# Kernel tuning notes

Measured on AMD Instinct MI355X. Metric: run time of the kernel, lower is better.

The kernel has to match this reference:

```python
import jax, jax.numpy as jnp
import numpy as np

B, P, D, H = 2048, 128, 64, 8
DB = 10  # D_obs + D_pos = 7 + 3, hard-coded in the module


def setup_inputs() -> dict:
    key = jax.random.key(0)
    ks = jax.random.split(key, 10)
    s = lambda fan_in: 1.0 / np.sqrt(fan_in)
    return {
        "x": jax.random.normal(ks[0], (B, D), dtype=jnp.float32),
        "b": jax.random.normal(ks[1], (B, P, DB), dtype=jnp.float32),
        "W_kvx": jax.random.uniform(ks[2], (D, 2 * H * D), jnp.float32, -s(D), s(D)),
        "b_kvx": jax.random.uniform(ks[3], (2 * H * D,), jnp.float32, -s(D), s(D)),
        "W_kvb": jax.random.uniform(ks[4], (DB, 2 * H * D), jnp.float32, -s(DB), s(DB)),
        "b_kvb": jax.random.uniform(ks[5], (2 * H * D,), jnp.float32, -s(DB), s(DB)),
        "W_q": jax.random.uniform(ks[6], (D, H * D), jnp.float32, -s(D), s(D)),
        "b_q": jax.random.uniform(ks[7], (H * D,), jnp.float32, -s(D), s(D)),
        "W_f": jax.random.uniform(ks[8], (H * D, D), jnp.float32, -s(H * D), s(H * D)),
        "b_f": jax.random.uniform(ks[9], (D,), jnp.float32, -s(H * D), s(H * D)),
    }


def reference(x, b, W_kvx, b_kvx, W_kvb, b_kvb, W_q, b_q, W_f, b_f):
    Bn, Dx = x.shape
    _, Pn, _ = b.shape
    # dual projections + broadcast add: [B,1,2HD] + [B,P,2HD]
    kv = (x @ W_kvx + b_kvx)[:, None, :] + (jnp.einsum('bpe,ef->bpf', b, W_kvb) + b_kvb)
    k, v = jnp.split(kv, 2, axis=-1)            # each [B,P,H*D]
    k = k.reshape(Bn, Pn, H, Dx)
    v = v.reshape(Bn, Pn, H, Dx)
    q = (x @ W_q + b_q).reshape(Bn, H, Dx)
    dots = jnp.einsum('bphd,bhd->bph', k, q) / np.sqrt(Dx).astype(np.float32)
    # NOTE: faithful to source — softmax over the HEAD axis (last dim of [B,P,H])
    attn = jax.nn.softmax(dots, axis=-1)
    vals = jnp.einsum('bph,bphd->bhd', attn, v)  # sum over positions P
    out = vals.reshape(Bn, H * Dx) @ W_f + b_f
    return out
```

## Files before the change

kernel.cpp:

```cpp
#include <hip/hip_runtime.h>

#define NDB 10

__global__ __launch_bounds__(256) void proj_kernel(
    const float* __restrict__ x, const float* __restrict__ W_kvx,
    const float* __restrict__ b_kvx, const float* __restrict__ b_kvb,
    const float* __restrict__ W_q, const float* __restrict__ b_q,
    float* __restrict__ XQ)
{
    __shared__ float x_t[64][68];
    const int t = threadIdx.x;
    const int row0 = blockIdx.x * 64;
    const int ct = blockIdx.y;

    {
        const int r = t & 63, kb = (t >> 6) * 16;
        float4 xv[4];
        #pragma unroll
        for (int i = 0; i < 4; ++i)
            xv[i] = *(const float4*)&x[(size_t)(row0 + r) * 64 + kb + i * 4];
        #pragma unroll
        for (int i = 0; i < 4; ++i) {
            x_t[kb + i * 4 + 0][r] = xv[i].x;
            x_t[kb + i * 4 + 1][r] = xv[i].y;
            x_t[kb + i * 4 + 2][r] = xv[i].z;
            x_t[kb + i * 4 + 3][r] = xv[i].w;
        }
    }
    __syncthreads();

    const bool iskv = (ct < 16);
    const int c0 = (iskv ? ct * 64 : (ct - 16) * 64) + (t & 15) * 4;
    const int stride = iskv ? 1024 : 512;
    const float* Wp = (iskv ? W_kvx : W_q) + c0;
    const int r0 = (t >> 4) * 4;

    float acc[4][4] = {};
    #pragma unroll 8
    for (int k = 0; k < 64; ++k) {
        float4 a  = *(const float4*)&x_t[k][r0];
        float4 wv = *(const float4*)&Wp[k * stride];
        float av[4] = {a.x, a.y, a.z, a.w};
        float wvv[4] = {wv.x, wv.y, wv.z, wv.w};
        #pragma unroll
        for (int i = 0; i < 4; ++i)
            #pragma unroll
            for (int jj = 0; jj < 4; ++jj)
                acc[i][jj] = fmaf(av[i], wvv[jj], acc[i][jj]);
    }
    float4 bias;
    if (iskv) {
        float4 b1 = *(const float4*)&b_kvx[c0];
        float4 b2 = *(const float4*)&b_kvb[c0];
        bias.x = b1.x + b2.x; bias.y = b1.y + b2.y;
        bias.z = b1.z + b2.z; bias.w = b1.w + b2.w;
    } else {
        bias = *(const float4*)&b_q[c0];
    }
    const int outcol = ct * 64 + (t & 15) * 4;
    #pragma unroll
    for (int i = 0; i < 4; ++i) {
        float4 o;
        o.x = acc[i][0] + bias.x; o.y = acc[i][1] + bias.y;
        o.z = acc[i][2] + bias.z; o.w = acc[i][3] + bias.w;
        *(float4*)&XQ[(size_t)(row0 + r0 + i) * 1536 + outcol] = o;
    }
}

__global__ __launch_bounds__(256) void attn_core(
    const float* __restrict__ bmat, const float* __restrict__ W_kvb,
    const float* __restrict__ XQ, float* __restrict__ VALS)
{
    __shared__ float bb_s[4][128][11];
    __shared__ float q_s[4][8][68];
    __shared__ float dot0_s[4][8];
    __shared__ float Wqkb_s[4][NDB][8];
    __shared__ float A_s[4][8];
    __shared__ float S_s[4][NDB][8];

    const int t = threadIdx.x, lane = t & 63, w = t >> 6;
    const int row = blockIdx.x * 4 + w;
    const float* __restrict__ xq = XQ + (size_t)row * 1536;

    {
        float4 a  = *(const float4*)&xq[1024 + lane * 4];
        float4 b4 = *(const float4*)&xq[1024 + 256 + lane * 4];
        int d0 = lane * 4;
        float av[4] = {a.x, a.y, a.z, a.w};
        float bv[4] = {b4.x, b4.y, b4.z, b4.w};
        #pragma unroll
        for (int c = 0; c < 4; ++c) {
            int d = d0 + c;
            q_s[w][d >> 6][d & 63] = av[c];
            int d2 = d + 256;
            q_s[w][d2 >> 6][d2 & 63] = bv[c];
        }
    }
    {
        const float* bsrc = bmat + (size_t)row * 1280;
        #pragma unroll
        for (int i = 0; i < 20; ++i) {
            int idx = lane + 64 * i;
            bb_s[w][idx / 10][idx % 10] = bsrc[idx];
        }
    }

    const int h = lane >> 3, i8 = lane & 7;
    {
        float s = 0.f;
        #pragma unroll
        for (int j = 0; j < 8; ++j) {
            int d = i8 + 8 * j;
            s = fmaf(xq[h * 64 + d], q_s[w][h][d], s);
        }
        s += __shfl_xor(s, 1); s += __shfl_xor(s, 2); s += __shfl_xor(s, 4);
        if (i8 == 0) dot0_s[w][h] = s;
    }
    #pragma unroll
    for (int e = 0; e < NDB; ++e) {
        float s = 0.f;
        #pragma unroll
        for (int m = 0; m < 8; ++m) {
            int d = i8 + 8 * m;
            s = fmaf(W_kvb[e * 1024 + h * 64 + d], q_s[w][h][d], s);
        }
        s += __shfl_xor(s, 1); s += __shfl_xor(s, 2); s += __shfl_xor(s, 4);
        if (i8 == 0) Wqkb_s[w][e][h] = s;
    }

    {
        const int hh = lane & 7, pg = lane >> 3;
        float aA = 0.f, aS[NDB];
        #pragma unroll
        for (int e = 0; e < NDB; ++e) aS[e] = 0.f;
        float wq[NDB];
        #pragma unroll
        for (int e = 0; e < NDB; ++e) wq[e] = Wqkb_s[w][e][hh];
        const float d0v = dot0_s[w][hh];
        #pragma unroll 4
        for (int it = 0; it < 16; ++it) {
            int p = pg + 8 * it;
            float bbv[NDB];
            #pragma unroll
            for (int e = 0; e < NDB; ++e) bbv[e] = bb_s[w][p][e];
            float dot = d0v;
            #pragma unroll
            for (int e = 0; e < NDB; ++e) dot = fmaf(bbv[e], wq[e], dot);
            dot *= 0.125f;
            float m = dot;
            m = fmaxf(m, __shfl_xor(m, 1));
            m = fmaxf(m, __shfl_xor(m, 2));
            m = fmaxf(m, __shfl_xor(m, 4));
            float ex = __expf(dot - m);
            float sum = ex;
            sum += __shfl_xor(sum, 1); sum += __shfl_xor(sum, 2); sum += __shfl_xor(sum, 4);
            float at = ex * __builtin_amdgcn_rcpf(sum);
            aA += at;
            #pragma unroll
            for (int e = 0; e < NDB; ++e) aS[e] = fmaf(at, bbv[e], aS[e]);
        }
        aA += __shfl_xor(aA, 8); aA += __shfl_xor(aA, 16); aA += __shfl_xor(aA, 32);
        #pragma unroll
        for (int e = 0; e < NDB; ++e) {
            aS[e] += __shfl_xor(aS[e], 8);
            aS[e] += __shfl_xor(aS[e], 16);
            aS[e] += __shfl_xor(aS[e], 32);
        }
        if (pg == 0) {
            A_s[w][hh] = aA;
            #pragma unroll
            for (int e = 0; e < NDB; ++e) S_s[w][e][hh] = aS[e];
        }
    }

    #pragma unroll
    for (int i = 0; i < 8; ++i) {
        int f = lane + 64 * i;
        float v = A_s[w][i] * xq[512 + f];
        #pragma unroll
        for (int e = 0; e < NDB; ++e)
            v = fmaf(S_s[w][e][i], W_kvb[e * 1024 + 512 + f], v);
        VALS[(size_t)row * 512 + f] = v;
    }
}

__global__ __launch_bounds__(256) void out_kernel(
    const float* __restrict__ VALS, const float* __restrict__ W_f,
    const float* __restrict__ b_f, float* __restrict__ out)
{
    __shared__ float wf_s[128][64];
    const int t = threadIdx.x, j = t & 63;
    const int row = blockIdx.x * 4 + (t >> 6);
    const int rowU = __builtin_amdgcn_readfirstlane(row);
    const float4* vrow = (const float4*)(VALS + (size_t)rowU * 512);

    float acc = 0.f;
    #pragma unroll
    for (int kt = 0; kt < 4; ++kt) {
        __syncthreads();
        #pragma unroll
        for (int i = 0; i < 8; ++i) {
            int fi = t + 256 * i;
            ((float4*)wf_s)[fi] = ((const float4*)(W_f + kt * 128 * 64))[fi];
        }
        __syncthreads();
        #pragma unroll 8
        for (int k4 = 0; k4 < 32; ++k4) {
            float4 v = vrow[kt * 32 + k4];
            int k = k4 * 4;
            acc = fmaf(v.x, wf_s[k + 0][j], acc);
            acc = fmaf(v.y, wf_s[k + 1][j], acc);
            acc = fmaf(v.z, wf_s[k + 2][j], acc);
            acc = fmaf(v.w, wf_s[k + 3][j], acc);
        }
    }
    out[(size_t)row * 64 + j] = acc + b_f[j];
}

extern "C" void kernel_launch(void* const* d_in, const int* in_sizes, int n_in,
                              void* d_out, int out_size, void* d_ws, size_t ws_size,
                              hipStream_t stream)
{
    const float* x     = (const float*)d_in[0];
    const float* bmat  = (const float*)d_in[1];
    const float* W_kvx = (const float*)d_in[2];
    const float* b_kvx = (const float*)d_in[3];
    const float* W_kvb = (const float*)d_in[4];
    const float* b_kvb = (const float*)d_in[5];
    const float* W_q   = (const float*)d_in[6];
    const float* b_q   = (const float*)d_in[7];
    const float* W_f   = (const float*)d_in[8];
    const float* b_f   = (const float*)d_in[9];
    float* out  = (float*)d_out;
    float* XQ   = (float*)d_ws;
    float* VALS = XQ + (size_t)2048 * 1536;

    proj_kernel<<<dim3(32, 24), 256, 0, stream>>>(x, W_kvx, b_kvx, b_kvb, W_q, b_q, XQ);
    attn_core<<<512, 256, 0, stream>>>(bmat, W_kvb, XQ, VALS);
    out_kernel<<<512, 256, 0, stream>>>(VALS, W_f, b_f, out);
}
```

Measured before the change: 131.6 us.

## Fuse output projection into attention kernel with one batch row per block

Merges out_kernel into attn_core, so VALS stays in shared memory instead of making a global write/read round trip, and one kernel launch goes away. Each block now handles a single batch row using all four wavefronts cooperatively: positions are split across waves, partial sums are reduced through shared memory, and the W_f GEMV is split over the K dimension with a final cross-wave sum. In exchange it adds several block-wide barriers, launches four times as many blocks, and reads W_f directly from global/cache for every row instead of staging it in LDS.

Result: faster. 109.2 us (-17.1%).

```diff
diff --git a/kernel.cpp b/kernel.cpp
--- a/kernel.cpp
+++ b/kernel.cpp
@@ -69,80 +69,80 @@
 
 __global__ __launch_bounds__(256) void attn_core(
     const float* __restrict__ bmat, const float* __restrict__ W_kvb,
-    const float* __restrict__ XQ, float* __restrict__ VALS)
+    const float* __restrict__ XQ, const float* __restrict__ W_f,
+    const float* __restrict__ b_f, float* __restrict__ out)
 {
-    __shared__ float bb_s[4][128][11];
-    __shared__ float q_s[4][8][68];
-    __shared__ float dot0_s[4][8];
-    __shared__ float Wqkb_s[4][NDB][8];
-    __shared__ float A_s[4][8];
-    __shared__ float S_s[4][NDB][8];
+    __shared__ float bb_s[128][11];
+    __shared__ float q_s[8][68];
+    __shared__ float dot0_s[8];
+    __shared__ float Wqkb_s[NDB][8];
+    __shared__ float partA[4][8];
+    __shared__ float partS[4][NDB][8];
+    __shared__ float A_s[8];
+    __shared__ float S_s[NDB][8];
+    __shared__ float vals_s[512];
+    __shared__ float pout[4][64];
 
     const int t = threadIdx.x, lane = t & 63, w = t >> 6;
-    const int row = blockIdx.x * 4 + w;
+    const int row = blockIdx.x;
     const float* __restrict__ xq = XQ + (size_t)row * 1536;
 
     {
-        float4 a  = *(const float4*)&xq[1024 + lane * 4];
-        float4 b4 = *(const float4*)&xq[1024 + 256 + lane * 4];
-        int d0 = lane * 4;
-        float av[4] = {a.x, a.y, a.z, a.w};
-        float bv[4] = {b4.x, b4.y, b4.z, b4.w};
-        #pragma unroll
-        for (int c = 0; c < 4; ++c) {
-            int d = d0 + c;
-            q_s[w][d >> 6][d & 63] = av[c];
-            int d2 = d + 256;
-            q_s[w][d2 >> 6][d2 & 63] = bv[c];
-        }
-    }
-    {
         const float* bsrc = bmat + (size_t)row * 1280;
         #pragma unroll
-        for (int i = 0; i < 20; ++i) {
-            int idx = lane + 64 * i;
-            bb_s[w][idx / 10][idx % 10] = bsrc[idx];
-        }
-    }
-
-    const int h = lane >> 3, i8 = lane & 7;
-    {
-        float s = 0.f;
-        #pragma unroll
-        for (int j = 0; j < 8; ++j) {
-            int d = i8 + 8 * j;
-            s = fmaf(xq[h * 64 + d], q_s[w][h][d], s);
-        }
-        s += __shfl_xor(s, 1); s += __shfl_xor(s, 2); s += __shfl_xor(s, 4);
-        if (i8 == 0) dot0_s[w][h] = s;
-    }
-    #pragma unroll
-    for (int e = 0; e < NDB; ++e) {
-        float s = 0.f;
-        #pragma unroll
-        for (int m = 0; m < 8; ++m) {
-            int d = i8 + 8 * m;
-            s = fmaf(W_kvb[e * 1024 + h * 64 + d], q_s[w][h][d], s);
-        }
-        s += __shfl_xor(s, 1); s += __shfl_xor(s, 2); s += __shfl_xor(s, 4);
-        if (i8 == 0) Wqkb_s[w][e][h] = s;
-    }
+        for (int i = 0; i < 5; ++i) {
+            int idx = t + 256 * i;
+            bb_s[idx / 10][idx % 10] = bsrc[idx];
+        }
+        float qa = xq[1024 + t];
+        float qb = xq[1024 + 256 + t];
+        q_s[t >> 6][t & 63] = qa;
+        q_s[(t + 256) >> 6][t & 63] = qb;
+        float p1 = xq[t] * qa;
+        float p2 = xq[t + 256] * qb;
+        #pragma unroll
+        for (int m = 1; m <= 32; m <<= 1) p1 += __shfl_xor(p1, m);
+        #pragma unroll
+        for (int m = 1; m <= 32; m <<= 1) p2 += __shfl_xor(p2, m);
+        if (lane == 0) { dot0_s[w] = p1; dot0_s[w + 4] = p2; }
+    }
+    __syncthreads();
+
+    {
+        const int g = t >> 3, l = t & 7;
+        #pragma unroll
+        for (int ro = 0; ro < 3; ++ro) {
+            int o = g + 32 * ro;
+            if (o < 80) {
+                int e = o >> 3, h = o & 7;
+                float s = 0.f;
+                #pragma unroll
+                for (int m = 0; m < 8; ++m) {
+                    int d = l + 8 * m;
+                    s = fmaf(W_kvb[e * 1024 + h * 64 + d], q_s[h][d], s);
+                }
+                s += __shfl_xor(s, 1); s += __shfl_xor(s, 2); s += __shfl_xor(s, 4);
+                if (l == 0) Wqkb_s[e][h] = s;
+            }
+        }
+    }
+    __syncthreads();
 
     {
         const int hh = lane & 7, pg = lane >> 3;
+        float wq[NDB];
+        #pragma unroll
+        for (int e = 0; e < NDB; ++e) wq[e] = Wqkb_s[e][hh];
+        const float d0v = dot0_s[hh];
         float aA = 0.f, aS[NDB];
         #pragma unroll
         for (int e = 0; e < NDB; ++e) aS[e] = 0.f;
-        float wq[NDB];
-        #pragma unroll
-        for (int e = 0; e < NDB; ++e) wq[e] = Wqkb_s[w][e][hh];
-        const float d0v = dot0_s[w][hh];
-        #pragma unroll 4
-        for (int it = 0; it < 16; ++it) {
-            int p = pg + 8 * it;
+        #pragma unroll
+        for (int it = 0; it < 4; ++it) {
+            int p = w * 32 + pg + 8 * it;
             float bbv[NDB];
             #pragma unroll
-            for (int e = 0; e < NDB; ++e) bbv[e] = bb_s[w][p][e];
+            for (int e = 0; e < NDB; ++e) bbv[e] = bb_s[p][e];
             float dot = d0v;
             #pragma unroll
             for (int e = 0; e < NDB; ++e) dot = fmaf(bbv[e], wq[e], dot);
@@ -167,54 +167,53 @@
             aS[e] += __shfl_xor(aS[e], 32);
         }
         if (pg == 0) {
-            A_s[w][hh] = aA;
-            #pragma unroll
-            for (int e = 0; e < NDB; ++e) S_s[w][e][hh] = aS[e];
-        }
-    }
-
-    #pragma unroll
-    for (int i = 0; i < 8; ++i) {
-        int f = lane + 64 * i;
-        float v = A_s[w][i] * xq[512 + f];
-        #pragma unroll
-        for (int e = 0; e < NDB; ++e)
-            v = fmaf(S_s[w][e][i], W_kvb[e * 1024 + 512 + f], v);
-        VALS[(size_t)row * 512 + f] = v;
-    }
-}
-
-__global__ __launch_bounds__(256) void out_kernel(
-    const float* __restrict__ VALS, const float* __restrict__ W_f,
-    const float* __restrict__ b_f, float* __restrict__ out)
-{
-    __shared__ float wf_s[128][64];
-    const int t = threadIdx.x, j = t & 63;
-    const int row = blockIdx.x * 4 + (t >> 6);
-    const int rowU = __builtin_amdgcn_readfirstlane(row);
-    const float4* vrow = (const float4*)(VALS + (size_t)rowU * 512);
-
-    float acc = 0.f;
-    #pragma unroll
-    for (int kt = 0; kt < 4; ++kt) {
-        __syncthreads();
-        #pragma unroll
-        for (int i = 0; i < 8; ++i) {
-            int fi = t + 256 * i;
-            ((float4*)wf_s)[fi] = ((const float4*)(W_f + kt * 128 * 64))[fi];
-        }
-        __syncthreads();
+            partA[w][hh] = aA;
+            #pragma unroll
+            for (int e = 0; e < NDB; ++e) partS[w][e][hh] = aS[e];
+        }
+    }
+    __syncthreads();
+
+    if (t < 8)  A_s[t] = partA[0][t] + partA[1][t] + partA[2][t] + partA[3][t];
+    if (t < 80) {
+        int e = t >> 3, h = t & 7;
+        S_s[e][h] = partS[0][e][h] + partS[1][e][h] + partS[2][e][h] + partS[3][e][h];
+    }
+    __syncthreads();
+
+    {
+        int f1 = t, f2 = t + 256;
+        float v1 = A_s[w] * xq[512 + f1];
+        float v2 = A_s[w + 4] * xq[512 + f2];
+        #pragma unroll
+        for (int e = 0; e < NDB; ++e) {
+            v1 = fmaf(S_s[e][w],     W_kvb[e * 1024 + 512 + f1], v1);
+            v2 = fmaf(S_s[e][w + 4], W_kvb[e * 1024 + 512 + f2], v2);
+        }
+        vals_s[f1] = v1;
+        vals_s[f2] = v2;
+    }
+    __syncthreads();
+
+    {
+        const int j = lane;
+        float acc = 0.f;
         #pragma unroll 8
         for (int k4 = 0; k4 < 32; ++k4) {
-            float4 v = vrow[kt * 32 + k4];
-            int k = k4 * 4;
-            acc = fmaf(v.x, wf_s[k + 0][j], acc);
-            acc = fmaf(v.y, wf_s[k + 1][j], acc);
-            acc = fmaf(v.z, wf_s[k + 2][j], acc);
-            acc = fmaf(v.w, wf_s[k + 3][j], acc);
-        }
-    }
-    out[(size_t)row * 64 + j] = acc + b_f[j];
+            int f = w * 128 + k4 * 4;
+            float4 v = *(const float4*)&vals_s[f];
+            acc = fmaf(v.x, W_f[(f + 0) * 64 + j], acc);
+            acc = fmaf(v.y, W_f[(f + 1) * 64 + j], acc);
+            acc = fmaf(v.z, W_f[(f + 2) * 64 + j], acc);
+            acc = fmaf(v.w, W_f[(f + 3) * 64 + j], acc);
+        }
+        pout[w][j] = acc;
+    }
+    __syncthreads();
+
+    if (t < 64)
+        out[(size_t)row * 64 + t] =
+            pout[0][t] + pout[1][t] + pout[2][t] + pout[3][t] + b_f[t];
 }
 
 extern "C" void kernel_launch(void* const* d_in, const int* in_sizes, int n_in,
@@ -231,11 +230,9 @@
     const float* b_q   = (const float*)d_in[7];
     const float* W_f   = (const float*)d_in[8];
     const float* b_f   = (const float*)d_in[9];
-    float* out  = (float*)d_out;
-    float* XQ   = (float*)d_ws;
-    float* VALS = XQ + (size_t)2048 * 1536;
+    float* out = (float*)d_out;
+    float* XQ  = (float*)d_ws;
 
     proj_kernel<<<dim3(32, 24), 256, 0, stream>>>(x, W_kvx, b_kvx, b_kvb, W_q, b_q, XQ);
-    attn_core<<<512, 256, 0, stream>>>(bmat, W_kvb, XQ, VALS);
-    out_kernel<<<512, 256, 0, stream>>>(VALS, W_f, b_f, out);
+    attn_core<<<2048, 256, 0, stream>>>(bmat, W_kvb, XQ, W_f, b_f, out);
 }
```
